# Optimization experiments

Measured on AMD Instinct MI355X. Metric: run time of the kernel, lower is better.

## Reference

```python
import math
import jax, jax.numpy as jnp
from jax import lax
import numpy as np

N = 512          # transform size; frame size = 2N
B = 16           # batch
T = 2048         # number of frames; signal length = N*T
PI = math.pi


def _make_mdct_filter(n: int, normalize: bool = True) -> jnp.ndarray:
    # filter[k, 0, t] = cos(pi/N * (t + 0.5 + N/2) * (k + 0.5)) / sqrt(N)
    k = jnp.arange(n, dtype=jnp.float32).reshape(n, 1, 1)
    t = jnp.arange(2 * n, dtype=jnp.float32).reshape(1, 1, 2 * n)
    f = jnp.cos(PI / n * (t + 0.5 + n / 2) * (k + 0.5))
    if normalize:
        f = f / jnp.sqrt(jnp.float32(n))
    return f  # [N, 1, 2N]


def setup_inputs() -> dict:
    key = jax.random.key(0)
    x = jax.random.normal(key, (B, 1, N * T), dtype=jnp.float32)
    mdct_filter = _make_mdct_filter(N, normalize=True)
    return {"x": x, "mdct_filter": mdct_filter}


def reference(x, mdct_filter):
    # Equivalent of F.conv1d(x, filter, stride=N, padding=N)
    n = mdct_filter.shape[0]
    # x: [B, 1, N*T] -> out: [B, N, T+1]
    out = lax.conv_general_dilated(
        x, mdct_filter,
        window_strides=(n,),
        padding=[(n, n)],
        dimension_numbers=("NCH", "OIH", "NCH"),
    )
    return out
```

## Files before the change

### kernel.cpp

```cpp
#include <hip/hip_runtime.h>
#include <hip/hip_bf16.h>
#include <stdint.h>
#include <stddef.h>


constexpr int N_ = 512;
constexpr int T_ = 2048;
constexpr int B_ = 16;
constexpr int LEN = N_ * T_;
constexpr int FRAMES = T_ + 1;
constexpr int COLS = B_ * FRAMES;
constexpr int NT_TILES = 257;
constexpr int KF = 512;
constexpr int BK = 64;

typedef __attribute__((ext_vector_type(8))) _Float16 f16x8;
typedef __attribute__((ext_vector_type(4))) _Float16 f16x4;
typedef __attribute__((ext_vector_type(4))) float f32x4;

#define GLD16(gptr, lptr)                                                     \
  __builtin_amdgcn_global_load_lds(                                           \
      (const __attribute__((address_space(1))) unsigned int*)(gptr),          \
      (__attribute__((address_space(3))) unsigned int*)(lptr), 16, 0, 0)

__global__ void prep_filter(const float* __restrict__ f,
                            _Float16* __restrict__ D) {
  int idx = (blockIdx.x * 256 + threadIdx.x) * 4;
  int k = idx >> 9;
  int j = idx & 511;
  int t = (j < 256) ? j : (j + 256);
  const float4 v = *(const float4*)&f[k * 1024 + t];
  f16x4 h = {(_Float16)v.x, (_Float16)v.y, (_Float16)v.z, (_Float16)v.w};
  *(f16x4*)&D[k * KF + j] = h;
}

__global__ __launch_bounds__(256, 3) void gemm_fused(
    const _Float16* __restrict__ D, const float* __restrict__ x,
    float* __restrict__ out) {
  __shared__ __align__(16) _Float16 As[128 * BK];
  __shared__ __align__(16) _Float16 Bs[128 * BK];

  const int id = blockIdx.x;
  const int xcd = id & 7;
  const int s = id >> 3;
  const int nt = (s >> 2) * 8 + xcd;
  if (nt >= NT_TILES) return;
  const int m0 = (s & 3) * 128;
  const int n0 = nt * 128;

  const int tid = threadIdx.x;
  const int wid = tid >> 6;
  const int lane = tid & 63;
  const int quad = lane >> 4;
  const int l16 = lane & 15;
  const int mw = (wid >> 1) * 64;
  const int nw = (wid & 1) * 64;

  const int rbase = tid >> 3;
  const int cch = tid & 7;
  const int swz = cch ^ (rbase & 7);
  int gg[4], lo[4];
  bool ok[4];
#pragma unroll
  for (int u = 0; u < 4; ++u) {
    int r = u * 32 + rbase;
    int col = n0 + r;
    int b = (int)((unsigned)col / (unsigned)FRAMES);
    int o = col - b * FRAMES;
    gg[u] = b * LEN + o * N_ - N_;
    lo[u] = b * LEN;
    ok[u] = (col < COLS);
  }

  f32x4 acc[4][4];
#pragma unroll
  for (int i = 0; i < 4; ++i)
#pragma unroll
    for (int j = 0; j < 4; ++j) acc[i][j] = (f32x4){0.f, 0.f, 0.f, 0.f};

  const _Float16* Dm = D + (size_t)m0 * KF;

  for (int kt = 0; kt < KF / BK; ++kt) {
    const int kb = kt * BK;
    __syncthreads();

#pragma unroll
    for (int u = 0; u < 4; ++u) {
      const int S = u * 256 + tid;
      const int rA = S >> 3;
      const int cA = (S & 7) ^ (rA & 7);
      GLD16(Dm + (size_t)rA * KF + kb + cA * 8, &As[S * 8]);
    }

    const int j0 = kb + cch * 8;
    const bool mi = (kb < 256);
    const int fo = mi ? j0 : (j0 + 256);
    const int ro = mi ? (504 - j0) : (1272 - j0);
    const float sgn = mi ? -1.0f : 1.0f;
#pragma unroll
    for (int u = 0; u < 4; ++u) {
      float4 a0 = {0.f, 0.f, 0.f, 0.f}, a1 = {0.f, 0.f, 0.f, 0.f};
      float4 r0 = {0.f, 0.f, 0.f, 0.f}, r1 = {0.f, 0.f, 0.f, 0.f};
      if (ok[u]) {
        const int fb = gg[u] + fo;
        const int rb = gg[u] + ro;
        if ((unsigned)(fb - lo[u]) <= (unsigned)(LEN - 8)) {
          a0 = *(const float4*)(x + fb);
          a1 = *(const float4*)(x + fb + 4);
        }
        if ((unsigned)(rb - lo[u]) <= (unsigned)(LEN - 8)) {
          r0 = *(const float4*)(x + rb);
          r1 = *(const float4*)(x + rb + 4);
        }
      }
      f16x8 h;
      h[0] = (_Float16)__builtin_fmaf(sgn, r1.w, a0.x);
      h[1] = (_Float16)__builtin_fmaf(sgn, r1.z, a0.y);
      h[2] = (_Float16)__builtin_fmaf(sgn, r1.y, a0.z);
      h[3] = (_Float16)__builtin_fmaf(sgn, r1.x, a0.w);
      h[4] = (_Float16)__builtin_fmaf(sgn, r0.w, a1.x);
      h[5] = (_Float16)__builtin_fmaf(sgn, r0.z, a1.y);
      h[6] = (_Float16)__builtin_fmaf(sgn, r0.y, a1.z);
      h[7] = (_Float16)__builtin_fmaf(sgn, r0.x, a1.w);
      const int r = u * 32 + rbase;
      *(f16x8*)&Bs[(r * 8 + swz) * 8] = h;
    }
    __syncthreads();

#pragma unroll
    for (int ko = 0; ko < 2; ++ko) {
      f16x8 af[4], bf[4];
#pragma unroll
      for (int i = 0; i < 4; ++i) {
        int ra = mw + i * 16 + l16;
        int rb = nw + i * 16 + l16;
        int ca = ko * 4 + quad;
        af[i] = *(const f16x8*)&As[(ra * 8 + (ca ^ (ra & 7))) * 8];
        bf[i] = *(const f16x8*)&Bs[(rb * 8 + (ca ^ (rb & 7))) * 8];
      }
#pragma unroll
      for (int i = 0; i < 4; ++i)
#pragma unroll
        for (int j = 0; j < 4; ++j)
          acc[i][j] = __builtin_amdgcn_mfma_f32_16x16x32_f16(af[i], bf[j], acc[i][j], 0, 0, 0);
    }
  }

#pragma unroll
  for (int i = 0; i < 4; ++i) {
#pragma unroll
    for (int j = 0; j < 4; ++j) {
      int col = n0 + nw + j * 16 + l16;
      if (col < COLS) {
        int b = col / FRAMES;
        int o = col - b * FRAMES;
        int rowb = m0 + mw + i * 16 + quad * 4;
        float* op = out + (size_t)b * N_ * FRAMES + (size_t)rowb * FRAMES + o;
#pragma unroll
        for (int r = 0; r < 4; ++r) op[(size_t)r * FRAMES] = acc[i][j][r];
      }
    }
  }
}

__global__ void naive_conv(const float* __restrict__ x, const float* __restrict__ f,
                           float* __restrict__ out) {
  int col = blockIdx.x;
  int k = threadIdx.x;
  __shared__ float win[1024];
  int b = col / FRAMES;
  int o = col - b * FRAMES;
  const float* xb = x + (size_t)b * LEN;
  int g = o * N_ - N_;
  for (int t = threadIdx.x; t < 1024; t += 512) {
    int i = g + t;
    win[t] = (i >= 0 && i < LEN) ? xb[i] : 0.0f;
  }
  __syncthreads();
  float s = 0.0f;
  const float* fk = f + (size_t)k * 1024;
  for (int t = 0; t < 1024; ++t) s += win[t] * fk[t];
  out[(size_t)b * N_ * FRAMES + (size_t)k * FRAMES + o] = s;
}

extern "C" void kernel_launch(void* const* d_in, const int* in_sizes, int n_in,
                              void* d_out, int out_size, void* d_ws, size_t ws_size,
                              hipStream_t stream) {
  const float* x = (const float*)d_in[0];
  const float* f = (const float*)d_in[1];
  float* out = (float*)d_out;

  const size_t need = (size_t)512 * 512 * sizeof(_Float16);
  if (ws_size < need) {
    naive_conv<<<COLS, 512, 0, stream>>>(x, f, out);
    return;
  }

  _Float16* D = (_Float16*)d_ws;
  prep_filter<<<256, 256, 0, stream>>>(f, D);
  gemm_fused<<<1056, 256, 0, stream>>>(D, x, out);
}
```

Baseline: 160.2 us.

## Double-buffer LDS tiles and prefetch next K-slice during MFMA compute

Halves the K tile to 32 and adds two LDS buffers for A and B. The next slice's filter copy (async global-to-LDS) and signal register loads are issued before the current slice's MFMAs, and the folded fp16 B tile is written to LDS afterwards. This overlaps global load latency with compute and cuts barriers to one per iteration. The cost is twice the loop iterations, more registers held for the prefetched signal values, and a different swizzle.

New measurement: 165.9 us. +3.6%, slower.

```diff
diff --git a/kernel.cpp b/kernel.cpp
--- a/kernel.cpp
+++ b/kernel.cpp
@@ -12,7 +12,8 @@
 constexpr int COLS = B_ * FRAMES;
 constexpr int NT_TILES = 257;
 constexpr int KF = 512;
-constexpr int BK = 64;
+constexpr int BK = 32;
+constexpr int KI = KF / BK;
 
 typedef __attribute__((ext_vector_type(8))) _Float16 f16x8;
 typedef __attribute__((ext_vector_type(4))) _Float16 f16x4;
@@ -37,15 +38,15 @@
 __global__ __launch_bounds__(256, 3) void gemm_fused(
     const _Float16* __restrict__ D, const float* __restrict__ x,
     float* __restrict__ out) {
-  __shared__ __align__(16) _Float16 As[128 * BK];
-  __shared__ __align__(16) _Float16 Bs[128 * BK];
+  __shared__ __align__(16) _Float16 As[2][128 * BK];
+  __shared__ __align__(16) _Float16 Bs[2][128 * BK];
 
   const int id = blockIdx.x;
   const int xcd = id & 7;
-  const int s = id >> 3;
-  const int nt = (s >> 2) * 8 + xcd;
+  const int sb = id >> 3;
+  const int nt = (sb >> 2) * 8 + xcd;
   if (nt >= NT_TILES) return;
-  const int m0 = (s & 3) * 128;
+  const int m0 = (sb & 3) * 128;
   const int n0 = nt * 128;
 
   const int tid = threadIdx.x;
@@ -56,21 +57,23 @@
   const int mw = (wid >> 1) * 64;
   const int nw = (wid & 1) * 64;
 
-  const int rbase = tid >> 3;
-  const int cch = tid & 7;
-  const int swz = cch ^ (rbase & 7);
-  int gg[4], lo[4];
-  bool ok[4];
-#pragma unroll
-  for (int u = 0; u < 4; ++u) {
-    int r = u * 32 + rbase;
-    int col = n0 + r;
+  const int cch = tid & 3;
+  const int rh = tid >> 2;
+  int gg[2], lo2[2], slotB[2];
+  bool ok2[2];
+#pragma unroll
+  for (int u = 0; u < 2; ++u) {
+    int row = rh + u * 64;
+    int col = n0 + row;
     int b = (int)((unsigned)col / (unsigned)FRAMES);
     int o = col - b * FRAMES;
     gg[u] = b * LEN + o * N_ - N_;
-    lo[u] = b * LEN;
-    ok[u] = (col < COLS);
-  }
+    lo2[u] = b * LEN;
+    ok2[u] = (col < COLS);
+    slotB[u] = row * 4 + (cch ^ (row & 3));
+  }
+
+  const _Float16* Dm = D + (size_t)m0 * KF;
 
   f32x4 acc[4][4];
 #pragma unroll
@@ -78,72 +81,86 @@
 #pragma unroll
     for (int j = 0; j < 4; ++j) acc[i][j] = (f32x4){0.f, 0.f, 0.f, 0.f};
 
-  const _Float16* Dm = D + (size_t)m0 * KF;
-
-  for (int kt = 0; kt < KF / BK; ++kt) {
-    const int kb = kt * BK;
-    __syncthreads();
-
-#pragma unroll
-    for (int u = 0; u < 4; ++u) {
-      const int S = u * 256 + tid;
-      const int rA = S >> 3;
-      const int cA = (S & 7) ^ (rA & 7);
-      GLD16(Dm + (size_t)rA * KF + kb + cA * 8, &As[S * 8]);
-    }
-
+  float4 qa0[2], qa1[2], qr0[2], qr1[2];
+
+  auto stageA = [&](int kb, int buf) {
+#pragma unroll
+    for (int u2 = 0; u2 < 2; ++u2) {
+      const int S = u2 * 256 + tid;
+      const int rA = S >> 2;
+      const int cA = (S & 3) ^ (rA & 3);
+      GLD16(Dm + (size_t)rA * KF + kb + cA * 8, &As[buf][S * 8]);
+    }
+  };
+  auto loadB = [&](int kb) {
+    const bool mi = (kb < 256);
     const int j0 = kb + cch * 8;
-    const bool mi = (kb < 256);
     const int fo = mi ? j0 : (j0 + 256);
     const int ro = mi ? (504 - j0) : (1272 - j0);
-    const float sgn = mi ? -1.0f : 1.0f;
-#pragma unroll
-    for (int u = 0; u < 4; ++u) {
-      float4 a0 = {0.f, 0.f, 0.f, 0.f}, a1 = {0.f, 0.f, 0.f, 0.f};
-      float4 r0 = {0.f, 0.f, 0.f, 0.f}, r1 = {0.f, 0.f, 0.f, 0.f};
-      if (ok[u]) {
+#pragma unroll
+    for (int u = 0; u < 2; ++u) {
+      qa0[u] = (float4){0.f, 0.f, 0.f, 0.f};
+      qa1[u] = (float4){0.f, 0.f, 0.f, 0.f};
+      qr0[u] = (float4){0.f, 0.f, 0.f, 0.f};
+      qr1[u] = (float4){0.f, 0.f, 0.f, 0.f};
+      if (ok2[u]) {
         const int fb = gg[u] + fo;
-        const int rb = gg[u] + ro;
-        if ((unsigned)(fb - lo[u]) <= (unsigned)(LEN - 8)) {
-          a0 = *(const float4*)(x + fb);
-          a1 = *(const float4*)(x + fb + 4);
+        const int rb2 = gg[u] + ro;
+        if ((unsigned)(fb - lo2[u]) <= (unsigned)(LEN - 8)) {
+          qa0[u] = *(const float4*)(x + fb);
+          qa1[u] = *(const float4*)(x + fb + 4);
         }
-        if ((unsigned)(rb - lo[u]) <= (unsigned)(LEN - 8)) {
-          r0 = *(const float4*)(x + rb);
-          r1 = *(const float4*)(x + rb + 4);
+        if ((unsigned)(rb2 - lo2[u]) <= (unsigned)(LEN - 8)) {
+          qr0[u] = *(const float4*)(x + rb2);
+          qr1[u] = *(const float4*)(x + rb2 + 4);
         }
       }
+    }
+  };
+  auto writeB = [&](int kb, int buf) {
+    const float sgn = (kb < 256) ? -1.0f : 1.0f;
+#pragma unroll
+    for (int u = 0; u < 2; ++u) {
       f16x8 h;
-      h[0] = (_Float16)__builtin_fmaf(sgn, r1.w, a0.x);
-      h[1] = (_Float16)__builtin_fmaf(sgn, r1.z, a0.y);
-      h[2] = (_Float16)__builtin_fmaf(sgn, r1.y, a0.z);
-      h[3] = (_Float16)__builtin_fmaf(sgn, r1.x, a0.w);
-      h[4] = (_Float16)__builtin_fmaf(sgn, r0.w, a1.x);
-      h[5] = (_Float16)__builtin_fmaf(sgn, r0.z, a1.y);
-      h[6] = (_Float16)__builtin_fmaf(sgn, r0.y, a1.z);
-      h[7] = (_Float16)__builtin_fmaf(sgn, r0.x, a1.w);
-      const int r = u * 32 + rbase;
-      *(f16x8*)&Bs[(r * 8 + swz) * 8] = h;
-    }
+      h[0] = (_Float16)__builtin_fmaf(sgn, qr1[u].w, qa0[u].x);
+      h[1] = (_Float16)__builtin_fmaf(sgn, qr1[u].z, qa0[u].y);
+      h[2] = (_Float16)__builtin_fmaf(sgn, qr1[u].y, qa0[u].z);
+      h[3] = (_Float16)__builtin_fmaf(sgn, qr1[u].x, qa0[u].w);
+      h[4] = (_Float16)__builtin_fmaf(sgn, qr0[u].w, qa1[u].x);
+      h[5] = (_Float16)__builtin_fmaf(sgn, qr0[u].z, qa1[u].y);
+      h[6] = (_Float16)__builtin_fmaf(sgn, qr0[u].y, qa1[u].z);
+      h[7] = (_Float16)__builtin_fmaf(sgn, qr0[u].x, qa1[u].w);
+      *(f16x8*)&Bs[buf][slotB[u] * 8] = h;
+    }
+  };
+
+  stageA(0, 0);
+  loadB(0);
+  writeB(0, 0);
+
+  for (int kt = 0; kt < KI; ++kt) {
+    const int cur = kt & 1;
+    const int nxt = cur ^ 1;
     __syncthreads();
-
-#pragma unroll
-    for (int ko = 0; ko < 2; ++ko) {
-      f16x8 af[4], bf[4];
-#pragma unroll
-      for (int i = 0; i < 4; ++i) {
-        int ra = mw + i * 16 + l16;
-        int rb = nw + i * 16 + l16;
-        int ca = ko * 4 + quad;
-        af[i] = *(const f16x8*)&As[(ra * 8 + (ca ^ (ra & 7))) * 8];
-        bf[i] = *(const f16x8*)&Bs[(rb * 8 + (ca ^ (rb & 7))) * 8];
-      }
-#pragma unroll
-      for (int i = 0; i < 4; ++i)
-#pragma unroll
-        for (int j = 0; j < 4; ++j)
-          acc[i][j] = __builtin_amdgcn_mfma_f32_16x16x32_f16(af[i], bf[j], acc[i][j], 0, 0, 0);
-    }
+    if (kt + 1 < KI) {
+      const int kbn = (kt + 1) * BK;
+      stageA(kbn, nxt);
+      loadB(kbn);
+    }
+    f16x8 af[4], bfr[4];
+#pragma unroll
+    for (int i = 0; i < 4; ++i) {
+      const int ra = mw + i * 16 + l16;
+      const int rb = nw + i * 16 + l16;
+      af[i] = *(const f16x8*)&As[cur][(ra * 4 + (quad ^ (ra & 3))) * 8];
+      bfr[i] = *(const f16x8*)&Bs[cur][(rb * 4 + (quad ^ (rb & 3))) * 8];
+    }
+#pragma unroll
+    for (int i = 0; i < 4; ++i)
+#pragma unroll
+      for (int j = 0; j < 4; ++j)
+        acc[i][j] = __builtin_amdgcn_mfma_f32_16x16x32_f16(af[i], bfr[j], acc[i][j], 0, 0, 0);
+    if (kt + 1 < KI) writeB((kt + 1) * BK, nxt);
   }
 
 #pragma unroll
```
